# Kernel optimization log

Hardware: AMD Instinct MI355X
Metric: run time of the kernel (lower is better)

## Reference

```python
import jax, jax.numpy as jnp
import numpy as np
from jax import lax

DIM = 768
HEADS = 12
EXPERTS = 4
CAPS = [0.4, 0.3, 0.2, 0.1]  # capacity fraction per expert e=0..E-1 (e=E-1 is the full-dim expert)
EPS = 1e-5


def _layernorm(x, g, b):
    mu = jnp.mean(x, axis=-1, keepdims=True)
    var = jnp.mean(jnp.square(x - mu), axis=-1, keepdims=True)
    return (x - mu) * lax.rsqrt(var + EPS) * g + b


def _route(x, router_w, router_b):
    # Expert-preferred capacity router: experts (largest dim first) greedily take
    # their top-capacity tokens by router probability among still-unassigned tokens.
    B, N, _ = x.shape
    probs = jax.nn.softmax(x @ router_w + router_b, axis=-1)  # [B,N,E]
    ks = [int(c * N) for c in CAPS]
    ks[-1] += N - sum(ks)  # remainder to the largest expert
    assigned = jnp.zeros((B, N), dtype=jnp.int32)
    avail = jnp.ones((B, N), dtype=bool)
    brow = jnp.arange(B)[:, None]
    for e in reversed(range(EXPERTS)):
        pe = jnp.where(avail, probs[:, :, e], -jnp.inf)
        _, idx = lax.top_k(pe, ks[e])  # [B, k_e]
        sel = jnp.zeros((B, N), dtype=bool).at[brow, idx].set(True)
        assigned = jnp.where(sel, e, assigned)
        avail = avail & ~sel
    router_probs = jnp.take_along_axis(probs, assigned[..., None], axis=-1)[..., 0]  # [B,N]
    return assigned, router_probs


def _feat_mask(token_mask, dtype):
    # expert e uses the first DIM / 2^(E-1-e) features (nested slicing)
    dims = jnp.array([DIM >> (EXPERTS - 1 - e) for e in range(EXPERTS)], dtype=jnp.int32)
    d_tok = dims[token_mask]  # [B,N]
    return (jnp.arange(DIM)[None, None, :] < d_tok[..., None]).astype(dtype)  # [B,N,D]


def _nested_attention(h, mask, wqkv, bqkv, wo, bo):
    # masking input + output of a full projection == using the top-left nested submatrix
    B, N, D = h.shape
    hd = D // HEADS
    qkv = ((h * mask) @ wqkv + bqkv) * jnp.tile(mask, (1, 1, 3))  # [B,N,3D]
    q, k, v = jnp.split(qkv, 3, axis=-1)
    q = q.reshape(B, N, HEADS, hd).transpose(0, 2, 1, 3)  # [B,H,N,hd]
    k = k.reshape(B, N, HEADS, hd).transpose(0, 2, 1, 3)
    v = v.reshape(B, N, HEADS, hd).transpose(0, 2, 1, 3)
    scores = jnp.einsum('bhqd,bhkd->bhqk', q, k) * (hd ** -0.5)
    attn = jax.nn.softmax(scores, axis=-1)
    out = jnp.einsum('bhqk,bhkd->bhqd', attn, v)  # [B,H,N,hd]
    out = out.transpose(0, 2, 1, 3).reshape(B, N, D) * mask
    return ((out @ wo) + bo) * mask


def setup_inputs() -> dict:
    key = jax.random.key(0)
    ks = jax.random.split(key, 8)
    B, N, D = 4, 1024, DIM
    s = 0.02
    return {
        'x': jax.random.normal(ks[0], (B, N, D), jnp.float32),
        'ln1_g': jnp.ones((D,), jnp.float32),
        'ln1_b': jnp.zeros((D,), jnp.float32),
        'router_w': jax.random.normal(ks[1], (D, EXPERTS), jnp.float32) * s,
        'router_b': jnp.zeros((EXPERTS,), jnp.float32),
        'wqkv': jax.random.normal(ks[2], (D, 3 * D), jnp.float32) * s,
        'bqkv': jnp.zeros((3 * D,), jnp.float32),
        'wo': jax.random.normal(ks[3], (D, D), jnp.float32) * s,
        'bo': jnp.zeros((D,), jnp.float32),
        'ln2_g': jnp.ones((D,), jnp.float32),
        'ln2_b': jnp.zeros((D,), jnp.float32),
        'w1': jax.random.normal(ks[4], (D, 4 * D), jnp.float32) * s,
        'b1': jnp.zeros((4 * D,), jnp.float32),
        'w2': jax.random.normal(ks[5], (4 * D, D), jnp.float32) * s,
        'b2': jnp.zeros((D,), jnp.float32),
    }


def reference(x, ln1_g, ln1_b, router_w, router_b, wqkv, bqkv, wo, bo,
              ln2_g, ln2_b, w1, b1, w2, b2):
    token_mask, router_probs = _route(x, router_w, router_b)
    mask = _feat_mask(token_mask, x.dtype)  # [B,N,D]
    z = x + _nested_attention(_layernorm(x, ln1_g, ln1_b), mask, wqkv, bqkv, wo, bo)
    h2 = _layernorm(z, ln2_g, ln2_b)
    z_prime = jax.nn.gelu(h2 @ w1 + b1, approximate=False) @ w2 + b2
    # probability-weighted token combine
    return z + router_probs[..., None] * z_prime
```

## Files before the change

kernel.cpp:

```cpp
#include <hip/hip_runtime.h>
#include <math.h>

#define DIM 768
#define NTOK 1024
#define BATCH 4
#define HEADS 12
#define TOKENS (BATCH * NTOK)

typedef __bf16 bf16;
typedef __attribute__((ext_vector_type(8))) __bf16 bf16x8;
typedef __attribute__((ext_vector_type(4))) float floatx4;

__global__ void router_kernel(const float* __restrict__ x,
                              const float* __restrict__ rw,
                              const float* __restrict__ rb,
                              float* __restrict__ probs) {
    int t = blockIdx.x;
    int tid = threadIdx.x;
    const float* xr = x + (size_t)t * DIM;
    double acc[4] = {0, 0, 0, 0};
    for (int k = tid; k < DIM; k += 256) {
        double xv = (double)xr[k];
        acc[0] += xv * (double)rw[k * 4 + 0];
        acc[1] += xv * (double)rw[k * 4 + 1];
        acc[2] += xv * (double)rw[k * 4 + 2];
        acc[3] += xv * (double)rw[k * 4 + 3];
    }
    __shared__ double red[256];
    __shared__ double logits[4];
    for (int e = 0; e < 4; ++e) {
        red[tid] = acc[e];
        __syncthreads();
        for (int s = 128; s > 0; s >>= 1) {
            if (tid < s) red[tid] += red[tid + s];
            __syncthreads();
        }
        if (tid == 0) logits[e] = red[0] + (double)rb[e];
        __syncthreads();
    }
    if (tid == 0) {
        double m = logits[0];
        for (int e = 1; e < 4; ++e) m = fmax(m, logits[e]);
        double s = 0.0, p[4];
        for (int e = 0; e < 4; ++e) { p[e] = exp(logits[e] - m); s += p[e]; }
        for (int e = 0; e < 4; ++e) probs[(size_t)t * 4 + e] = (float)(p[e] / s);
    }
}

__global__ __launch_bounds__(1024) void route_kernel(const float* __restrict__ probs,
                                                     int* __restrict__ dtok_g,
                                                     float* __restrict__ rprobs_g) {
    int b = blockIdx.x;
    int tid = threadIdx.x;
    __shared__ float sp[1024];
    __shared__ int si[1024];
    __shared__ int s_av[1024];
    __shared__ int s_as[1024];
    s_av[tid] = 1;
    s_as[tid] = 0;
    const int ks_e[4] = {409, 307, 204, 104};
    const float* pb = probs + (size_t)b * NTOK * 4;
    for (int e = 3; e >= 1; --e) {
        __syncthreads();
        sp[tid] = s_av[tid] ? pb[tid * 4 + e] : -INFINITY;
        si[tid] = tid;
        for (int size = 2; size <= 1024; size <<= 1) {
            for (int stride = size >> 1; stride > 0; stride >>= 1) {
                __syncthreads();
                int i = tid, j = i ^ stride;
                if (j > i) {
                    float pi = sp[i], pj = sp[j];
                    int ii = si[i], ij = si[j];
                    bool up = ((i & size) == 0);
                    bool before = (pi > pj) || (pi == pj && ii < ij);
                    if (up != before) { sp[i] = pj; sp[j] = pi; si[i] = ij; si[j] = ii; }
                }
            }
        }
        __syncthreads();
        if (tid < ks_e[e]) {
            int tok = si[tid];
            s_as[tok] = e;
            s_av[tok] = 0;
        }
    }
    __syncthreads();
    int a = s_as[tid];
    dtok_g[b * NTOK + tid] = DIM >> (3 - a);
    rprobs_g[b * NTOK + tid] = pb[tid * 4 + a];
}

__global__ void ln_mask_kernel(const float* __restrict__ x,
                               const float* __restrict__ g,
                               const float* __restrict__ bta,
                               const int* __restrict__ dtok,
                               bf16* __restrict__ out) {
    int t = blockIdx.x;
    int tid = threadIdx.x;
    const float* xr = x + (size_t)t * DIM;
    float s = 0.0f;
    for (int k = tid; k < DIM; k += 256) s += xr[k];
    __shared__ float red[256];
    red[tid] = s;
    __syncthreads();
    for (int st = 128; st > 0; st >>= 1) {
        if (tid < st) red[tid] += red[tid + st];
        __syncthreads();
    }
    float mu = red[0] / DIM;
    __syncthreads();
    float v = 0.0f;
    for (int k = tid; k < DIM; k += 256) { float d = xr[k] - mu; v += d * d; }
    red[tid] = v;
    __syncthreads();
    for (int st = 128; st > 0; st >>= 1) {
        if (tid < st) red[tid] += red[tid + st];
        __syncthreads();
    }
    float rs = rsqrtf(red[0] / DIM + 1e-5f);
    int d = dtok ? dtok[t] : DIM;
    for (int k = tid; k < DIM; k += 256) {
        float val = (xr[k] - mu) * rs * g[k] + bta[k];
        out[(size_t)t * DIM + k] = (bf16)((k < d) ? val : 0.0f);
    }
}

__global__ __launch_bounds__(256) void transpose_bf16_kernel(const float* __restrict__ W,
                                                             bf16* __restrict__ Wt,
                                                             int K, int N) {
    __shared__ float t[32][33];
    int bx = blockIdx.x * 32;
    int by = blockIdx.y * 32;
    int tx = threadIdx.x, ty = threadIdx.y;
#pragma unroll
    for (int i = 0; i < 4; ++i)
        t[ty + i * 8][tx] = W[(size_t)(by + ty + i * 8) * N + bx + tx];
    __syncthreads();
#pragma unroll
    for (int i = 0; i < 4; ++i)
        Wt[(size_t)(bx + ty + i * 8) * K + by + tx] = (bf16)t[tx][ty + i * 8];
}

#define LDT 40
template <int MODE>
__global__ __launch_bounds__(256) void gemm_mfma(const bf16* __restrict__ A,
                                                 const bf16* __restrict__ Bt,
                                                 const float* __restrict__ bias,
                                                 void* __restrict__ Cout,
                                                 int M, int NN, int K,
                                                 const int* __restrict__ dtok,
                                                 const float* __restrict__ aux,
                                                 const float* __restrict__ rp) {
    __shared__ bf16 As[128 * LDT];
    __shared__ bf16 Bs[128 * LDT];
    int n0 = blockIdx.x * 128;
    int m0 = blockIdx.y * 128;
    int tid = threadIdx.x;
    int wv = tid >> 6;
    int lane = tid & 63;
    int l16 = lane & 15, q4 = lane >> 4;
    int wm = (wv >> 1) * 64, wn = (wv & 1) * 64;
    floatx4 acc[4][4] = {};
    for (int k0 = 0; k0 < K; k0 += 32) {
        __syncthreads();
#pragma unroll
        for (int s = tid; s < 512; s += 256) {
            int row = s >> 2, part = s & 3;
            *(floatx4*)&As[row * LDT + part * 8] =
                *(const floatx4*)&A[(size_t)(m0 + row) * K + k0 + part * 8];
            *(floatx4*)&Bs[row * LDT + part * 8] =
                *(const floatx4*)&Bt[(size_t)(n0 + row) * K + k0 + part * 8];
        }
        __syncthreads();
        bf16x8 af[4], bfr[4];
#pragma unroll
        for (int t = 0; t < 4; ++t) {
            af[t] = *(const bf16x8*)&As[(wm + t * 16 + l16) * LDT + q4 * 8];
            bfr[t] = *(const bf16x8*)&Bs[(wn + t * 16 + l16) * LDT + q4 * 8];
        }
#pragma unroll
        for (int i = 0; i < 4; ++i)
#pragma unroll
            for (int j = 0; j < 4; ++j)
                acc[i][j] = __builtin_amdgcn_mfma_f32_16x16x32_bf16(af[i], bfr[j], acc[i][j], 0, 0, 0);
    }
#pragma unroll
    for (int i = 0; i < 4; ++i) {
#pragma unroll
        for (int j = 0; j < 4; ++j) {
            int col = n0 + wn + j * 16 + l16;
#pragma unroll
            for (int r = 0; r < 4; ++r) {
                int row = m0 + wm + i * 16 + q4 * 4 + r;
                float c = acc[i][j][r] + bias[col];
                if (MODE == 0) {
                    int jm = col % 768;
                    c = (jm < dtok[row]) ? c : 0.0f;
                    ((bf16*)Cout)[(size_t)row * NN + col] = (bf16)c;
                } else if (MODE == 1) {
                    c = (col < dtok[row]) ? c : 0.0f;
                    c += aux[(size_t)row * NN + col];
                    ((float*)Cout)[(size_t)row * NN + col] = c;
                } else if (MODE == 2) {
                    c = 0.5f * c * (1.0f + erff(c * 0.70710678118654752f));
                    ((bf16*)Cout)[(size_t)row * NN + col] = (bf16)c;
                } else {
                    c = aux[(size_t)row * NN + col] + rp[row] * c;
                    ((float*)Cout)[(size_t)row * NN + col] = c;
                }
            }
        }
    }
}

#define LDH 72
__global__ __launch_bounds__(256) void attn_mfma(const bf16* __restrict__ qkv,
                                                 const int* __restrict__ dtok,
                                                 bf16* __restrict__ attno) {
    int qt = blockIdx.x;
    int h = blockIdx.y;
    int b = blockIdx.z;
    int tid = threadIdx.x;
    int wv = tid >> 6;
    int lane = tid & 63;
    int l16 = lane & 15, q4 = lane >> 4;
    __shared__ bf16 Qs[64 * LDH];
    __shared__ bf16 Ks[64 * LDH];
    __shared__ bf16 Vt[64 * LDH];
    __shared__ bf16 Ps[4][16 * LDH];
    size_t base = (size_t)b * NTOK * 2304;
    for (int s = tid; s < 512; s += 256) {
        int row = s >> 3, part = s & 7;
        *(floatx4*)&Qs[row * LDH + part * 8] =
            *(const floatx4*)&qkv[base + (size_t)(qt * 64 + row) * 2304 + h * 64 + part * 8];
    }
    floatx4 o[4] = {};
    float m_r[4] = {-INFINITY, -INFINITY, -INFINITY, -INFINITY};
    float l_r[4] = {0.0f, 0.0f, 0.0f, 0.0f};
    for (int kt = 0; kt < 16; ++kt) {
        __syncthreads();
        for (int s = tid; s < 512; s += 256) {
            int row = s >> 3, part = s & 7;
            *(floatx4*)&Ks[row * LDH + part * 8] =
                *(const floatx4*)&qkv[base + (size_t)(kt * 64 + row) * 2304 + 768 + h * 64 + part * 8];
            floatx4 vv =
                *(const floatx4*)&qkv[base + (size_t)(kt * 64 + row) * 2304 + 1536 + h * 64 + part * 8];
            const bf16* vp = (const bf16*)&vv;
#pragma unroll
            for (int j = 0; j < 8; ++j) Vt[(part * 8 + j) * LDH + row] = vp[j];
        }
        __syncthreads();
        floatx4 sc[4] = {};
#pragma unroll
        for (int ch = 0; ch < 2; ++ch) {
            bf16x8 aq = *(const bf16x8*)&Qs[(wv * 16 + l16) * LDH + ch * 32 + q4 * 8];
#pragma unroll
            for (int nt = 0; nt < 4; ++nt) {
                bf16x8 bk = *(const bf16x8*)&Ks[(nt * 16 + l16) * LDH + ch * 32 + q4 * 8];
                sc[nt] = __builtin_amdgcn_mfma_f32_16x16x32_bf16(aq, bk, sc[nt], 0, 0, 0);
            }
        }
        float alpha[4], psum[4];
#pragma unroll
        for (int r = 0; r < 4; ++r) {
            float v0 = fmaxf(fmaxf(sc[0][r], sc[1][r]), fmaxf(sc[2][r], sc[3][r])) * 0.125f;
#pragma unroll
            for (int msk = 1; msk < 16; msk <<= 1) v0 = fmaxf(v0, __shfl_xor(v0, msk));
            float mn = fmaxf(m_r[r], v0);
            alpha[r] = __expf(m_r[r] - mn);
            m_r[r] = mn;
            psum[r] = 0.0f;
        }
#pragma unroll
        for (int nt = 0; nt < 4; ++nt)
#pragma unroll
            for (int r = 0; r < 4; ++r) {
                float p = __expf(sc[nt][r] * 0.125f - m_r[r]);
                psum[r] += p;
                Ps[wv][(q4 * 4 + r) * LDH + nt * 16 + l16] = (bf16)p;
            }
#pragma unroll
        for (int r = 0; r < 4; ++r) {
            float s = psum[r];
#pragma unroll
            for (int msk = 1; msk < 16; msk <<= 1) s += __shfl_xor(s, msk);
            l_r[r] = l_r[r] * alpha[r] + s;
        }
#pragma unroll
        for (int dt = 0; dt < 4; ++dt)
#pragma unroll
            for (int r = 0; r < 4; ++r) o[dt][r] *= alpha[r];
        __syncthreads();
#pragma unroll
        for (int ch = 0; ch < 2; ++ch) {
            bf16x8 ap = *(const bf16x8*)&Ps[wv][l16 * LDH + ch * 32 + q4 * 8];
#pragma unroll
            for (int dt = 0; dt < 4; ++dt) {
                bf16x8 bv = *(const bf16x8*)&Vt[(dt * 16 + l16) * LDH + ch * 32 + q4 * 8];
                o[dt] = __builtin_amdgcn_mfma_f32_16x16x32_bf16(ap, bv, o[dt], 0, 0, 0);
            }
        }
    }
#pragma unroll
    for (int r = 0; r < 4; ++r) {
        int tokrow = qt * 64 + wv * 16 + q4 * 4 + r;
        int dt_tok = dtok[b * NTOK + tokrow];
        float inv = 1.0f / l_r[r];
#pragma unroll
        for (int dt = 0; dt < 4; ++dt) {
            int col = h * 64 + dt * 16 + l16;
            float val = (col < dt_tok) ? o[dt][r] * inv : 0.0f;
            attno[((size_t)b * NTOK + tokrow) * DIM + col] = (bf16)val;
        }
    }
}

extern "C" void kernel_launch(void* const* d_in, const int* in_sizes, int n_in,
                              void* d_out, int out_size, void* d_ws, size_t ws_size,
                              hipStream_t stream) {
    const float* x = (const float*)d_in[0];
    const float* ln1g = (const float*)d_in[1];
    const float* ln1b = (const float*)d_in[2];
    const float* rw = (const float*)d_in[3];
    const float* rb = (const float*)d_in[4];
    const float* wqkv = (const float*)d_in[5];
    const float* bqkv = (const float*)d_in[6];
    const float* wo = (const float*)d_in[7];
    const float* bo = (const float*)d_in[8];
    const float* ln2g = (const float*)d_in[9];
    const float* ln2b = (const float*)d_in[10];
    const float* w1 = (const float*)d_in[11];
    const float* b1 = (const float*)d_in[12];
    const float* w2 = (const float*)d_in[13];
    const float* b2 = (const float*)d_in[14];
    float* out = (float*)d_out;

    char* ws = (char*)d_ws;
    size_t off = 0;
    auto alloc = [&](size_t bytes) {
        void* p = ws + off;
        off = (off + bytes + 255) & ~(size_t)255;
        return p;
    };
    bf16* h1m = (bf16*)alloc(sizeof(bf16) * TOKENS * DIM);
    float* probs = (float*)alloc(sizeof(float) * TOKENS * 4);
    float* rprobs = (float*)alloc(sizeof(float) * TOKENS);
    int* dtok = (int*)alloc(sizeof(int) * TOKENS);
    bf16* qkvb = (bf16*)alloc(sizeof(bf16) * TOKENS * 3 * DIM);
    bf16* attno = (bf16*)alloc(sizeof(bf16) * TOKENS * DIM);
    float* z = (float*)alloc(sizeof(float) * TOKENS * DIM);
    bf16* h2 = (bf16*)alloc(sizeof(bf16) * TOKENS * DIM);
    bf16* ffn1 = (bf16*)alloc(sizeof(bf16) * TOKENS * 4 * DIM);
    bf16* wqkvT = (bf16*)alloc(sizeof(bf16) * DIM * 3 * DIM);
    bf16* woT = (bf16*)alloc(sizeof(bf16) * DIM * DIM);
    bf16* w1T = (bf16*)alloc(sizeof(bf16) * DIM * 4 * DIM);
    bf16* w2T = (bf16*)alloc(sizeof(bf16) * 4 * DIM * DIM);

    dim3 tb(32, 8);
    transpose_bf16_kernel<<<dim3(2304 / 32, 768 / 32), tb, 0, stream>>>(wqkv, wqkvT, 768, 2304);
    transpose_bf16_kernel<<<dim3(768 / 32, 768 / 32), tb, 0, stream>>>(wo, woT, 768, 768);
    transpose_bf16_kernel<<<dim3(3072 / 32, 768 / 32), tb, 0, stream>>>(w1, w1T, 768, 3072);
    transpose_bf16_kernel<<<dim3(768 / 32, 3072 / 32), tb, 0, stream>>>(w2, w2T, 3072, 768);

    router_kernel<<<TOKENS, 256, 0, stream>>>(x, rw, rb, probs);
    route_kernel<<<BATCH, 1024, 0, stream>>>(probs, dtok, rprobs);
    ln_mask_kernel<<<TOKENS, 256, 0, stream>>>(x, ln1g, ln1b, dtok, h1m);
    gemm_mfma<0><<<dim3(2304 / 128, 4096 / 128), 256, 0, stream>>>(
        h1m, wqkvT, bqkv, qkvb, TOKENS, 2304, 768, dtok, nullptr, nullptr);
    attn_mfma<<<dim3(16, 12, 4), 256, 0, stream>>>(qkvb, dtok, attno);
    gemm_mfma<1><<<dim3(768 / 128, 4096 / 128), 256, 0, stream>>>(
        attno, woT, bo, z, TOKENS, 768, 768, dtok, x, nullptr);
    ln_mask_kernel<<<TOKENS, 256, 0, stream>>>(z, ln2g, ln2b, nullptr, h2);
    gemm_mfma<2><<<dim3(3072 / 128, 4096 / 128), 256, 0, stream>>>(
        h2, w1T, b1, ffn1, TOKENS, 3072, 768, nullptr, nullptr, nullptr);
    gemm_mfma<3><<<dim3(768 / 128, 4096 / 128), 256, 0, stream>>>(
        ffn1, w2T, b2, out, TOKENS, 768, 3072, nullptr, z, rprobs);
}
```

Before: 424.0 us.

## Double-buffer GEMM tiles, split-K the FFN2 GEMM, and rank-count routing

The GEMM kernel now keeps two LDS buffers and prefetches the next K tile into registers while MFMAs run on the current one, halving the barriers per K step. The FFN2 GEMM (K=3072, only 192 blocks) is split along K into two slices that write fp32 partials, and a new reduce kernel sums them and applies bias, router-prob scaling and the residual. This adds parallelism for that GEMM at the cost of extra partial traffic and one more launch. The routing bitonic sort is replaced by a per-thread O(N) rank count against shared memory, which removes the many syncthreads stages.

```diff
diff --git a/kernel.cpp b/kernel.cpp
--- a/kernel.cpp
+++ b/kernel.cpp
@@ -53,41 +53,24 @@
     int b = blockIdx.x;
     int tid = threadIdx.x;
     __shared__ float sp[1024];
-    __shared__ int si[1024];
-    __shared__ int s_av[1024];
-    __shared__ int s_as[1024];
-    s_av[tid] = 1;
-    s_as[tid] = 0;
     const int ks_e[4] = {409, 307, 204, 104};
     const float* pb = probs + (size_t)b * NTOK * 4;
+    int avail = 1, assigned = 0;
     for (int e = 3; e >= 1; --e) {
         __syncthreads();
-        sp[tid] = s_av[tid] ? pb[tid * 4 + e] : -INFINITY;
-        si[tid] = tid;
-        for (int size = 2; size <= 1024; size <<= 1) {
-            for (int stride = size >> 1; stride > 0; stride >>= 1) {
-                __syncthreads();
-                int i = tid, j = i ^ stride;
-                if (j > i) {
-                    float pi = sp[i], pj = sp[j];
-                    int ii = si[i], ij = si[j];
-                    bool up = ((i & size) == 0);
-                    bool before = (pi > pj) || (pi == pj && ii < ij);
-                    if (up != before) { sp[i] = pj; sp[j] = pi; si[i] = ij; si[j] = ii; }
-                }
-            }
-        }
-        __syncthreads();
-        if (tid < ks_e[e]) {
-            int tok = si[tid];
-            s_as[tok] = e;
-            s_av[tok] = 0;
-        }
-    }
-    __syncthreads();
-    int a = s_as[tid];
-    dtok_g[b * NTOK + tid] = DIM >> (3 - a);
-    rprobs_g[b * NTOK + tid] = pb[tid * 4 + a];
+        float pi = avail ? pb[tid * 4 + e] : -INFINITY;
+        sp[tid] = pi;
+        __syncthreads();
+        int cnt = 0;
+#pragma unroll 4
+        for (int j = 0; j < 1024; ++j) {
+            float pj = sp[j];
+            cnt += (pj > pi) || (pj == pi && j < tid);
+        }
+        if (avail && cnt < ks_e[e]) { assigned = e; avail = 0; }
+    }
+    dtok_g[b * NTOK + tid] = DIM >> (3 - assigned);
+    rprobs_g[b * NTOK + tid] = pb[tid * 4 + assigned];
 }
 
 __global__ void ln_mask_kernel(const float* __restrict__ x,
@@ -147,42 +130,71 @@
                                                  const bf16* __restrict__ Bt,
                                                  const float* __restrict__ bias,
                                                  void* __restrict__ Cout,
-                                                 int M, int NN, int K,
+                                                 int M, int NN, int K, int Kc,
                                                  const int* __restrict__ dtok,
                                                  const float* __restrict__ aux,
                                                  const float* __restrict__ rp) {
-    __shared__ bf16 As[128 * LDT];
-    __shared__ bf16 Bs[128 * LDT];
+    __shared__ bf16 As[2][128 * LDT];
+    __shared__ bf16 Bs[2][128 * LDT];
     int n0 = blockIdx.x * 128;
     int m0 = blockIdx.y * 128;
+    int kbase = blockIdx.z * Kc;
     int tid = threadIdx.x;
     int wv = tid >> 6;
     int lane = tid & 63;
     int l16 = lane & 15, q4 = lane >> 4;
     int wm = (wv >> 1) * 64, wn = (wv & 1) * 64;
+    const bf16* Ap = A + (size_t)m0 * K + kbase;
+    const bf16* Bp = Bt + (size_t)n0 * K + kbase;
+    floatx4 pa[2], pb[2];
+#pragma unroll
+    for (int u = 0; u < 2; ++u) {
+        int s = tid + u * 256, row = s >> 2, part = s & 3;
+        pa[u] = *(const floatx4*)&Ap[(size_t)row * K + part * 8];
+        pb[u] = *(const floatx4*)&Bp[(size_t)row * K + part * 8];
+    }
+#pragma unroll
+    for (int u = 0; u < 2; ++u) {
+        int s = tid + u * 256, row = s >> 2, part = s & 3;
+        *(floatx4*)&As[0][row * LDT + part * 8] = pa[u];
+        *(floatx4*)&Bs[0][row * LDT + part * 8] = pb[u];
+    }
+    __syncthreads();
     floatx4 acc[4][4] = {};
-    for (int k0 = 0; k0 < K; k0 += 32) {
-        __syncthreads();
-#pragma unroll
-        for (int s = tid; s < 512; s += 256) {
-            int row = s >> 2, part = s & 3;
-            *(floatx4*)&As[row * LDT + part * 8] =
-                *(const floatx4*)&A[(size_t)(m0 + row) * K + k0 + part * 8];
-            *(floatx4*)&Bs[row * LDT + part * 8] =
-                *(const floatx4*)&Bt[(size_t)(n0 + row) * K + k0 + part * 8];
-        }
-        __syncthreads();
+    int kIters = Kc / 32;
+    int cur = 0;
+    for (int it = 0; it < kIters; ++it) {
+        bool notlast = (it + 1 < kIters);
+        if (notlast) {
+            int ko = (it + 1) * 32;
+#pragma unroll
+            for (int u = 0; u < 2; ++u) {
+                int s = tid + u * 256, row = s >> 2, part = s & 3;
+                pa[u] = *(const floatx4*)&Ap[(size_t)row * K + ko + part * 8];
+                pb[u] = *(const floatx4*)&Bp[(size_t)row * K + ko + part * 8];
+            }
+        }
         bf16x8 af[4], bfr[4];
 #pragma unroll
         for (int t = 0; t < 4; ++t) {
-            af[t] = *(const bf16x8*)&As[(wm + t * 16 + l16) * LDT + q4 * 8];
-            bfr[t] = *(const bf16x8*)&Bs[(wn + t * 16 + l16) * LDT + q4 * 8];
+            af[t] = *(const bf16x8*)&As[cur][(wm + t * 16 + l16) * LDT + q4 * 8];
+            bfr[t] = *(const bf16x8*)&Bs[cur][(wn + t * 16 + l16) * LDT + q4 * 8];
         }
 #pragma unroll
         for (int i = 0; i < 4; ++i)
 #pragma unroll
             for (int j = 0; j < 4; ++j)
                 acc[i][j] = __builtin_amdgcn_mfma_f32_16x16x32_bf16(af[i], bfr[j], acc[i][j], 0, 0, 0);
+        if (notlast) {
+#pragma unroll
+            for (int u = 0; u < 2; ++u) {
+                int s = tid + u * 256, row = s >> 2, part = s & 3;
+                *(floatx4*)&As[cur ^ 1][row * LDT + part * 8] = pa[u];
+                *(floatx4*)&Bs[cur ^ 1][row * LDT + part * 8] = pb[u];
+            }
+            __syncthreads();
+            cur ^= 1;
+        }
     }
 #pragma unroll
     for (int i = 0; i < 4; ++i) {
@@ -192,6 +204,11 @@
 #pragma unroll
             for (int r = 0; r < 4; ++r) {
                 int row = m0 + wm + i * 16 + q4 * 4 + r;
+                if (MODE == 4) {
+                    ((float*)Cout)[(size_t)blockIdx.z * M * NN + (size_t)row * NN + col] =
+                        acc[i][j][r];
+                    continue;
+                }
                 float c = acc[i][j][r] + bias[col];
                 if (MODE == 0) {
                     int jm = col % 768;
@@ -204,13 +221,30 @@
                 } else if (MODE == 2) {
                     c = 0.5f * c * (1.0f + erff(c * 0.70710678118654752f));
                     ((bf16*)Cout)[(size_t)row * NN + col] = (bf16)c;
-                } else {
+                } else if (MODE == 3) {
                     c = aux[(size_t)row * NN + col] + rp[row] * c;
                     ((float*)Cout)[(size_t)row * NN + col] = c;
                 }
             }
         }
     }
+}
+
+__global__ __launch_bounds__(256) void ffn2_reduce(const float* __restrict__ part,
+                                                   const float* __restrict__ z,
+                                                   const float* __restrict__ bias,
+                                                   const float* __restrict__ rp,
+                                                   float* __restrict__ out) {
+    size_t idx = ((size_t)blockIdx.x * 256 + threadIdx.x) * 4;
+    int row = (int)(idx / DIM);
+    int col = (int)(idx % DIM);
+    floatx4 p0 = *(const floatx4*)&part[idx];
+    floatx4 p1 = *(const floatx4*)&part[(size_t)TOKENS * DIM + idx];
+    floatx4 zz = *(const floatx4*)&z[idx];
+    floatx4 bb = *(const floatx4*)&bias[col];
+    float r = rp[row];
+    floatx4 o = zz + (p0 + p1 + bb) * r;
+    *(floatx4*)&out[idx] = o;
 }
 
 #define LDH 72
@@ -355,6 +389,7 @@
     bf16* woT = (bf16*)alloc(sizeof(bf16) * DIM * DIM);
     bf16* w1T = (bf16*)alloc(sizeof(bf16) * DIM * 4 * DIM);
     bf16* w2T = (bf16*)alloc(sizeof(bf16) * 4 * DIM * DIM);
+    float* part = (float*)alloc(sizeof(float) * 2 * TOKENS * DIM);
 
     dim3 tb(32, 8);
     transpose_bf16_kernel<<<dim3(2304 / 32, 768 / 32), tb, 0, stream>>>(wqkv, wqkvT, 768, 2304);
@@ -366,13 +401,14 @@
     route_kernel<<<BATCH, 1024, 0, stream>>>(probs, dtok, rprobs);
     ln_mask_kernel<<<TOKENS, 256, 0, stream>>>(x, ln1g, ln1b, dtok, h1m);
     gemm_mfma<0><<<dim3(2304 / 128, 4096 / 128), 256, 0, stream>>>(
-        h1m, wqkvT, bqkv, qkvb, TOKENS, 2304, 768, dtok, nullptr, nullptr);
+        h1m, wqkvT, bqkv, qkvb, TOKENS, 2304, 768, 768, dtok, nullptr, nullptr);
     attn_mfma<<<dim3(16, 12, 4), 256, 0, stream>>>(qkvb, dtok, attno);
     gemm_mfma<1><<<dim3(768 / 128, 4096 / 128), 256, 0, stream>>>(
-        attno, woT, bo, z, TOKENS, 768, 768, dtok, x, nullptr);
+        attno, woT, bo, z, TOKENS, 768, 768, 768, dtok, x, nullptr);
     ln_mask_kernel<<<TOKENS, 256, 0, stream>>>(z, ln2g, ln2b, nullptr, h2);
     gemm_mfma<2><<<dim3(3072 / 128, 4096 / 128), 256, 0, stream>>>(
-        h2, w1T, b1, ffn1, TOKENS, 3072, 768, nullptr, nullptr, nullptr);
-    gemm_mfma<3><<<dim3(768 / 128, 4096 / 128), 256, 0, stream>>>(
-        ffn1, w2T, b2, out, TOKENS, 768, 3072, nullptr, z, rprobs);
-}
+        h2, w1T, b1, ffn1, TOKENS, 3072, 768, 768, nullptr, nullptr, nullptr);
+    gemm_mfma<4><<<dim3(768 / 128, 4096 / 128, 2), 256, 0, stream>>>(
+        ffn1, w2T, nullptr, part, TOKENS, 768, 3072, 1536, nullptr, nullptr, nullptr);
+    ffn2_reduce<<<TOKENS * DIM / 1024, 256, 0, stream>>>(part, z, b2, rprobs, out);
+}
```

Measured after the change: 456.9 us. 7.7% more time.
